# Kernel optimization log

Hardware: AMD Instinct MI355X
Metric: run time of the kernel (lower is better)

## Reference

```python
import jax, jax.numpy as jnp
import numpy as np


def _bilinear_gather(corr, x, y):
    # corr: [N, H2, W2]; x, y: [N, K, K] pixel coords; zero padding outside,
    # matching F.grid_sample(mode='bilinear', padding_mode='zeros', align_corners=True).
    N, H2, W2 = corr.shape
    corr_flat = corr.reshape(N, H2 * W2)
    x0 = jnp.floor(x)
    y0 = jnp.floor(y)
    wx1 = x - x0
    wy1 = y - y0

    def gather(xi, yi):
        valid = (xi >= 0) & (xi <= W2 - 1) & (yi >= 0) & (yi <= H2 - 1)
        xc = jnp.clip(xi, 0, W2 - 1).astype(jnp.int32)
        yc = jnp.clip(yi, 0, H2 - 1).astype(jnp.int32)
        idx = (yc * W2 + xc).reshape(N, -1)
        vals = jnp.take_along_axis(corr_flat, idx, axis=1).reshape(xi.shape)
        return jnp.where(valid, vals, jnp.zeros((), corr.dtype))

    return (gather(x0, y0) * (1 - wx1) * (1 - wy1)
            + gather(x0 + 1, y0) * wx1 * (1 - wy1)
            + gather(x0, y0 + 1) * (1 - wx1) * wy1
            + gather(x0 + 1, y0 + 1) * wx1 * wy1)


def setup_inputs() -> dict:
    key = jax.random.key(0)
    k1, k2, k3 = jax.random.split(key, 3)
    B, D, H, W = 2, 256, 64, 64
    fmap1 = jax.random.normal(k1, (B, D, H, W), dtype=jnp.float32)
    fmap2 = jax.random.normal(k2, (B, D, H, W), dtype=jnp.float32)
    # coords in pixel space [0, W-1]
    coords = jax.random.uniform(k3, (B, 2, H, W), dtype=jnp.float32) * (W - 1)
    return {"fmap1": fmap1, "fmap2": fmap2, "coords": coords, "radius": 4}


def reference(fmap1, fmap2, coords, radius):
    B, D, H, W = fmap1.shape
    # all-pairs correlation: [B, H*W, H*W], scaled by 1/sqrt(D)
    f1 = fmap1.reshape(B, D, H * W)
    f2 = fmap2.reshape(B, D, H * W)
    corr = jnp.einsum('bdn,bdm->bnm', f1, f2) / jnp.sqrt(jnp.asarray(D, jnp.float32))
    corr = corr.reshape(B * H * W, H, W)

    r = radius
    K = 2 * r + 1
    d = jnp.linspace(-r, r, K, dtype=jnp.float32)
    dyg, dxg = jnp.meshgrid(d, d, indexing='ij')
    delta = jnp.stack([dyg, dxg], axis=-1)  # [K, K, 2] (matches torch.meshgrid(dy, dx))

    centroid = coords.transpose(0, 2, 3, 1).reshape(B * H * W, 1, 1, 2)
    coords_lvl = centroid + delta[None]  # [N, K, K, 2]
    # RAFT bilinear_sampler: channel 0 is x, channel 1 is y
    x = coords_lvl[..., 0]
    y = coords_lvl[..., 1]

    out = _bilinear_gather(corr, x, y)  # [N, K, K]
    out = out.reshape(B, H, W, K * K).transpose(0, 3, 1, 2)
    return out.astype(jnp.float32)
```

## Files before the change

kernel.cpp:

```cpp
#include <hip/hip_runtime.h>

#define HWC 4096
#define WC 64
#define HC 64
#define DC 256
#define BC 2
#define KKC 81

typedef _Float16 h2 __attribute__((ext_vector_type(2)));
typedef _Float16 h8 __attribute__((ext_vector_type(8)));

static __device__ inline float dot8(h8 v, h8 a, float s) {
#if __has_builtin(__builtin_amdgcn_fdot2)
    s = __builtin_amdgcn_fdot2((h2){v[0], v[1]}, (h2){a[0], a[1]}, s, false);
    s = __builtin_amdgcn_fdot2((h2){v[2], v[3]}, (h2){a[2], a[3]}, s, false);
    s = __builtin_amdgcn_fdot2((h2){v[4], v[5]}, (h2){a[4], a[5]}, s, false);
    s = __builtin_amdgcn_fdot2((h2){v[6], v[7]}, (h2){a[6], a[7]}, s, false);
#else
#pragma unroll
    for (int k = 0; k < 8; ++k) s += (float)v[k] * (float)a[k];
#endif
    return s;
}

#define DPP_ADD(x, ctrl) \
    ((x) + __int_as_float(__builtin_amdgcn_update_dpp(0, __float_as_int(x), (ctrl), 0xF, 0xF, true)))

__global__ __launch_bounds__(256) void transpose_h_k(const float* __restrict__ f1,
                                                     const float* __restrict__ f2,
                                                     _Float16* __restrict__ o1,
                                                     _Float16* __restrict__ o2) {
    __shared__ float tile[64][33];
    const int z = blockIdx.z;
    const int b = z & 1;
    const float* in = (z >> 1) ? f2 : f1;
    _Float16* out = (z >> 1) ? o2 : o1;
    in += (size_t)b * DC * HWC;
    out += (size_t)b * HWC * DC;

    const int m0 = blockIdx.x * 32, d0 = blockIdx.y * 64;
    const int tid = threadIdx.x;
    const int tx = tid & 31, ty = tid >> 5;
#pragma unroll
    for (int k = 0; k < 8; ++k)
        tile[ty + k * 8][tx] = in[(size_t)(d0 + ty + k * 8) * HWC + m0 + tx];
    __syncthreads();

    const int dx = tid & 7, my = tid >> 3;
    h8 v;
#pragma unroll
    for (int e = 0; e < 8; ++e) v[e] = (_Float16)tile[dx * 8 + e][my];
    *(h8*)(out + (size_t)(m0 + my) * DC + d0 + dx * 8) = v;
}

__global__ __launch_bounds__(1024) void sort_k(const float* __restrict__ coords,
                                               int* __restrict__ sorted) {
    __shared__ int hist[64];
    __shared__ int base[64];
    const int b = blockIdx.x;
    const int tid = threadIdx.x;
    if (tid < 64) hist[tid] = 0;
    __syncthreads();
    int key[4];
#pragma unroll
    for (int k = 0; k < 4; ++k) {
        const int hw = tid * 4 + k;
        const float y = coords[((size_t)b * 2 + 1) * HWC + hw];
        key[k] = min(max((int)floorf(y), 0), 63);
        atomicAdd(&hist[key[k]], 1);
    }
    __syncthreads();
    if (tid == 0) {
        int acc = 0;
        for (int i = 0; i < 64; ++i) { base[i] = acc; acc += hist[i]; }
    }
    __syncthreads();
#pragma unroll
    for (int k = 0; k < 4; ++k) {
        const int hw = tid * 4 + k;
        const int pos = atomicAdd(&base[key[k]], 1);
        sorted[b * HWC + pos] = hw;
    }
}

__global__ __launch_bounds__(256) void corr_k(const _Float16* __restrict__ f1t,
                                              const _Float16* __restrict__ f2t,
                                              const float* __restrict__ coords,
                                              const int* __restrict__ sorted,
                                              float* __restrict__ out) {
    __shared__ float Cs[112];

    const int bid = blockIdx.x;
    const int x8 = bid & 7;
    const int b = x8 >> 2;
    const int q = x8 & 3;
    const int s = bid >> 3;
    const int hw = sorted[b * HWC + q * 1024 + s];

    const int tid = threadIdx.x;
    const int g = tid >> 4;
    const int l = tid & 15;

    const float x = coords[((size_t)b * 2 + 0) * HWC + hw];
    const float y = coords[((size_t)b * 2 + 1) * HWC + hw];
    const float x0f = floorf(x), y0f = floorf(y);
    const float wx = x - x0f, wy = y - y0f;
    const int ix0 = (int)x0f, iy0 = (int)y0f;

    const h8* ap = (const h8*)f1t + ((size_t)(b * HWC + hw)) * 32 + l * 2;
    const h8 a0 = ap[0], a1 = ap[1];
    const h8* f2b = (const h8*)f2t + (size_t)b * HWC * 32;

    h8 v0[7], v1[7];
    float vm[7];
#pragma unroll
    for (int it = 0; it < 7; ++it) {
        int t = it * 16 + g;
        t = t > 99 ? 99 : t;
        const int yi = t / 10, xi = t - yi * 10;
        const int gy = iy0 - 4 + yi, gx = ix0 - 4 + xi;
        const bool valid = ((unsigned)gy < (unsigned)HC) & ((unsigned)gx < (unsigned)WC);
        const int gyc = min(max(gy, 0), HC - 1);
        const int gxc = min(max(gx, 0), WC - 1);
        const h8* vp = f2b + (size_t)(gyc * WC + gxc) * 32 + l * 2;
        v0[it] = vp[0];
        v1[it] = vp[1];
        vm[it] = valid ? 0.0625f : 0.f;
    }

#pragma unroll
    for (int it = 0; it < 7; ++it) {
        float s2 = dot8(v0[it], a0, 0.f);
        s2 = dot8(v1[it], a1, s2);
        s2 *= vm[it];
        s2 = DPP_ADD(s2, 0xB1);
        s2 = DPP_ADD(s2, 0x4E);
        s2 = DPP_ADD(s2, 0x124);
        s2 = DPP_ADD(s2, 0x128);
        const int t = it * 16 + g;
        if (l == 0 && t < 100) Cs[t] = s2;
    }
    __syncthreads();

    if (tid < KKC) {
        const int i = tid / 9, j = tid % 9;
        const float w00 = (1.f - wx) * (1.f - wy);
        const float w01 = wx * (1.f - wy);
        const float w10 = (1.f - wx) * wy;
        const float w11 = wx * wy;
        const float r = w00 * Cs[j * 10 + i]       + w01 * Cs[j * 10 + i + 1] +
                        w10 * Cs[(j + 1) * 10 + i] + w11 * Cs[(j + 1) * 10 + i + 1];
        out[((size_t)(b * KKC + tid)) * HWC + hw] = r;
    }
}

extern "C" void kernel_launch(void* const* d_in, const int* in_sizes, int n_in,
                              void* d_out, int out_size, void* d_ws, size_t ws_size,
                              hipStream_t stream) {
    const float* fmap1 = (const float*)d_in[0];
    const float* fmap2 = (const float*)d_in[1];
    const float* coords = (const float*)d_in[2];
    float* out = (float*)d_out;

    const size_t perH = (size_t)BC * HWC * DC;
    _Float16* f1t = (_Float16*)d_ws;
    _Float16* f2t = f1t + perH;
    int* sorted = (int*)(f2t + perH);

    transpose_h_k<<<dim3(HWC / 32, DC / 64, 4), dim3(256), 0, stream>>>(fmap1, fmap2, f1t, f2t);
    sort_k<<<dim3(BC), dim3(1024), 0, stream>>>(coords, sorted);
    corr_k<<<dim3(BC * HWC), dim3(256), 0, stream>>>(f1t, f2t, coords, sorted, out);
}
```

Measured before the change: 97.34 us.

## Bin queries into 2D spatial cells and stage shared fmap2 patch in LDS

Queries are now sorted into 8x16 spatial cells (by x/8 and y/4) instead of by row. Each block owns one cell and loads a 13x17-pixel fmap2 halo patch into shared memory once. Each wave then handles one query at a time, reading its 10x10 neighbourhood from LDS instead of global memory. This cuts redundant global gathers, at the cost of a large LDS footprint, one block per CU, only 256 blocks, and load imbalance when cells hold uneven query counts.

```diff
diff --git a/kernel.cpp b/kernel.cpp
--- a/kernel.cpp
+++ b/kernel.cpp
@@ -6,6 +6,9 @@
 #define DC 256
 #define BC 2
 #define KKC 81
+#define NBIN 128
+#define SLOTS 221
+#define SLOT_H 264
 
 typedef _Float16 h2 __attribute__((ext_vector_type(2)));
 typedef _Float16 h8 __attribute__((ext_vector_type(8)));
@@ -54,103 +57,131 @@
 }
 
 __global__ __launch_bounds__(1024) void sort_k(const float* __restrict__ coords,
-                                               int* __restrict__ sorted) {
-    __shared__ int hist[64];
-    __shared__ int base[64];
+                                               int* __restrict__ sorted,
+                                               int* __restrict__ off) {
+    __shared__ int hist[NBIN];
+    __shared__ int base[NBIN];
     const int b = blockIdx.x;
     const int tid = threadIdx.x;
-    if (tid < 64) hist[tid] = 0;
+    if (tid < NBIN) hist[tid] = 0;
     __syncthreads();
     int key[4];
 #pragma unroll
     for (int k = 0; k < 4; ++k) {
         const int hw = tid * 4 + k;
+        const float x = coords[((size_t)b * 2 + 0) * HWC + hw];
         const float y = coords[((size_t)b * 2 + 1) * HWC + hw];
-        key[k] = min(max((int)floorf(y), 0), 63);
+        const int cx = min(max((int)floorf(x), 0), 63) >> 3;
+        const int cy = min(max((int)floorf(y), 0), 63) >> 2;
+        key[k] = cy * 8 + cx;
         atomicAdd(&hist[key[k]], 1);
     }
     __syncthreads();
     if (tid == 0) {
         int acc = 0;
-        for (int i = 0; i < 64; ++i) { base[i] = acc; acc += hist[i]; }
-    }
+        for (int i = 0; i < NBIN; ++i) { base[i] = acc; acc += hist[i]; }
+    }
+    __syncthreads();
+    if (tid < NBIN) off[b * (NBIN + 1) + tid] = base[tid];
+    if (tid == 0) off[b * (NBIN + 1) + NBIN] = HWC;
     __syncthreads();
 #pragma unroll
     for (int k = 0; k < 4; ++k) {
-        const int hw = tid * 4 + k;
         const int pos = atomicAdd(&base[key[k]], 1);
-        sorted[b * HWC + pos] = hw;
-    }
-}
-
-__global__ __launch_bounds__(256) void corr_k(const _Float16* __restrict__ f1t,
-                                              const _Float16* __restrict__ f2t,
-                                              const float* __restrict__ coords,
-                                              const int* __restrict__ sorted,
-                                              float* __restrict__ out) {
-    __shared__ float Cs[112];
+        sorted[b * HWC + pos] = tid * 4 + k;
+    }
+}
+
+__global__ __launch_bounds__(256, 1) void corr_k(const _Float16* __restrict__ f1t,
+                                                 const _Float16* __restrict__ f2t,
+                                                 const float* __restrict__ coords,
+                                                 const int* __restrict__ sorted,
+                                                 const int* __restrict__ off,
+                                                 float* __restrict__ out) {
+    __shared__ _Float16 patch[SLOTS * SLOT_H];
+    __shared__ float Cs[4][112];
 
     const int bid = blockIdx.x;
-    const int x8 = bid & 7;
-    const int b = x8 >> 2;
-    const int q = x8 & 3;
-    const int s = bid >> 3;
-    const int hw = sorted[b * HWC + q * 1024 + s];
-
+    const int b = bid >> 7, cell = bid & 127;
+    const int cy = cell >> 3, cx = cell & 7;
+    const int oy = cy * 4 - 4, ox = cx * 8 - 4;
     const int tid = threadIdx.x;
-    const int g = tid >> 4;
-    const int l = tid & 15;
-
-    const float x = coords[((size_t)b * 2 + 0) * HWC + hw];
-    const float y = coords[((size_t)b * 2 + 1) * HWC + hw];
-    const float x0f = floorf(x), y0f = floorf(y);
-    const float wx = x - x0f, wy = y - y0f;
-    const int ix0 = (int)x0f, iy0 = (int)y0f;
-
-    const h8* ap = (const h8*)f1t + ((size_t)(b * HWC + hw)) * 32 + l * 2;
-    const h8 a0 = ap[0], a1 = ap[1];
+
     const h8* f2b = (const h8*)f2t + (size_t)b * HWC * 32;
-
-    h8 v0[7], v1[7];
-    float vm[7];
-#pragma unroll
-    for (int it = 0; it < 7; ++it) {
-        int t = it * 16 + g;
-        t = t > 99 ? 99 : t;
-        const int yi = t / 10, xi = t - yi * 10;
-        const int gy = iy0 - 4 + yi, gx = ix0 - 4 + xi;
-        const bool valid = ((unsigned)gy < (unsigned)HC) & ((unsigned)gx < (unsigned)WC);
-        const int gyc = min(max(gy, 0), HC - 1);
-        const int gxc = min(max(gx, 0), WC - 1);
-        const h8* vp = f2b + (size_t)(gyc * WC + gxc) * 32 + l * 2;
-        v0[it] = vp[0];
-        v1[it] = vp[1];
-        vm[it] = valid ? 0.0625f : 0.f;
-    }
-
-#pragma unroll
-    for (int it = 0; it < 7; ++it) {
-        float s2 = dot8(v0[it], a0, 0.f);
-        s2 = dot8(v1[it], a1, s2);
-        s2 *= vm[it];
-        s2 = DPP_ADD(s2, 0xB1);
-        s2 = DPP_ADD(s2, 0x4E);
-        s2 = DPP_ADD(s2, 0x124);
-        s2 = DPP_ADD(s2, 0x128);
-        const int t = it * 16 + g;
-        if (l == 0 && t < 100) Cs[t] = s2;
-    }
-    __syncthreads();
-
-    if (tid < KKC) {
-        const int i = tid / 9, j = tid % 9;
+    {
+        const int sl = tid >> 4, l16 = tid & 15;
+        for (int s = sl; s < SLOTS; s += 16) {
+            const int ly = s / 17, lx = s - ly * 17;
+            const int gy = min(max(oy + ly, 0), HC - 1);
+            const int gx = min(max(ox + lx, 0), WC - 1);
+            const h8* src = f2b + (size_t)(gy * WC + gx) * 32 + l16 * 2;
+            const h8 u0 = src[0], u1 = src[1];
+            h8* dst = (h8*)(patch + s * SLOT_H) + l16 * 2;
+            dst[0] = u0; dst[1] = u1;
+        }
+    }
+    const int start = off[b * (NBIN + 1) + cell];
+    const int end   = off[b * (NBIN + 1) + cell + 1];
+    __syncthreads();
+
+    const int wv = tid >> 6, l = tid & 63;
+    const int g = (tid >> 4) & 3, il = tid & 15;
+
+    for (int p = start + wv; p < end; p += 4) {
+        const int hw = sorted[b * HWC + p];
+        const float x = coords[((size_t)b * 2 + 0) * HWC + hw];
+        const float y = coords[((size_t)b * 2 + 1) * HWC + hw];
+        const float x0f = floorf(x), y0f = floorf(y);
+        const float wx = x - x0f, wy = y - y0f;
+        const int ix0 = (int)x0f, iy0 = (int)y0f;
+        const int dy = iy0 - 4 - oy;
+        const int dx = ix0 - 4 - ox;
+
+        const _Float16* f1c = f1t + ((size_t)(b * HWC) + hw) * DC;
+        const h8 a0 = *(const h8*)(f1c + il * 8);
+        const h8 a1 = *(const h8*)(f1c + 128 + il * 8);
+
+#pragma unroll
+        for (int i = 0; i < 25; ++i) {
+            const int t = g * 25 + i;
+            const int yi = t / 10, xi = t - yi * 10;
+            const int slot = (dy + yi) * 17 + (dx + xi);
+            const _Float16* pp = patch + slot * SLOT_H + il * 8;
+            const h8 v0 = *(const h8*)pp;
+            const h8 v1 = *(const h8*)(pp + 128);
+            const int gy = iy0 - 4 + yi, gx = ix0 - 4 + xi;
+            const float vm = (((unsigned)gy < (unsigned)HC) &
+                              ((unsigned)gx < (unsigned)WC)) ? 0.0625f : 0.f;
+            float s = dot8(v0, a0, 0.f);
+            s = dot8(v1, a1, s);
+            s *= vm;
+            s = DPP_ADD(s, 0xB1);
+            s = DPP_ADD(s, 0x4E);
+            s = DPP_ADD(s, 0x124);
+            s = DPP_ADD(s, 0x128);
+            if (il == 0) Cs[wv][t] = s;
+        }
+#if __has_builtin(__builtin_amdgcn_wave_barrier)
+        __builtin_amdgcn_wave_barrier();
+#else
+        __builtin_amdgcn_sched_barrier(0);
+#endif
         const float w00 = (1.f - wx) * (1.f - wy);
         const float w01 = wx * (1.f - wy);
         const float w10 = (1.f - wx) * wy;
         const float w11 = wx * wy;
-        const float r = w00 * Cs[j * 10 + i]       + w01 * Cs[j * 10 + i + 1] +
-                        w10 * Cs[(j + 1) * 10 + i] + w11 * Cs[(j + 1) * 10 + i + 1];
-        out[((size_t)(b * KKC + tid)) * HWC + hw] = r;
+        {
+            const int k = l, i = k / 9, j = k - (k / 9) * 9;
+            const float r = w00 * Cs[wv][j * 10 + i]       + w01 * Cs[wv][j * 10 + i + 1] +
+                            w10 * Cs[wv][(j + 1) * 10 + i] + w11 * Cs[wv][(j + 1) * 10 + i + 1];
+            out[((size_t)(b * KKC + k)) * HWC + hw] = r;
+        }
+        if (l < KKC - 64) {
+            const int k = 64 + l, i = k / 9, j = k - (k / 9) * 9;
+            const float r = w00 * Cs[wv][j * 10 + i]       + w01 * Cs[wv][j * 10 + i + 1] +
+                            w10 * Cs[wv][(j + 1) * 10 + i] + w11 * Cs[wv][(j + 1) * 10 + i + 1];
+            out[((size_t)(b * KKC + k)) * HWC + hw] = r;
+        }
     }
 }
 
@@ -166,8 +197,9 @@
     _Float16* f1t = (_Float16*)d_ws;
     _Float16* f2t = f1t + perH;
     int* sorted = (int*)(f2t + perH);
+    int* off = sorted + BC * HWC;
 
     transpose_h_k<<<dim3(HWC / 32, DC / 64, 4), dim3(256), 0, stream>>>(fmap1, fmap2, f1t, f2t);
-    sort_k<<<dim3(BC), dim3(1024), 0, stream>>>(coords, sorted);
-    corr_k<<<dim3(BC * HWC), dim3(256), 0, stream>>>(f1t, f2t, coords, sorted, out);
-}
+    sort_k<<<dim3(BC), dim3(1024), 0, stream>>>(coords, sorted, off);
+    corr_k<<<dim3(BC * NBIN), dim3(256), 0, stream>>>(f1t, f2t, coords, sorted, off, out);
+}
```

Result: slower. 119.0 us (+22.2%).
